# Optimization experiments

Measured on AMD Instinct MI355X. Metric: run time of the kernel, lower is better.

The kernel has to match this reference:

```python
import jax, jax.numpy as jnp
import numpy as np

# ---- static config (mirrors init_kwargs) ----
WIN_X, WIN_Y = 12, 12
GRID_X, GRID_Y = 468, 468
BATCH = 4
SHIFTS = ((0, 0), (6, 6))
MAX_WIN_X = GRID_X // WIN_X + 1            # 40
MAX_WIN_Y = GRID_Y // WIN_Y + 1            # 40
MAX_WIN_PER_SAMPLE = MAX_WIN_X * MAX_WIN_Y # 1600
# (level, max_tokens, drop_range_lo, drop_range_hi)
DROP_INFO = ((0, 30, 0, 30), (1, 60, 30, 60), (2, 100, 60, 100000))
SENTINEL = 2_000_000_000  # window id for masked-out voxels (sorts to the end)


def _window_partition(coors):
    # coors: [N,4] = [b, z, y, x] int32 -> batch-unique window index per shift
    out = []
    for sx, sy in SHIFTS:
        x = coors[:, 3] + sx
        y = coors[:, 2] + sy
        wx = x // WIN_X
        wy = y // WIN_Y
        out.append((coors[:, 0] * MAX_WIN_PER_SAMPLE + wx * MAX_WIN_Y + wy).astype(jnp.int32))
    return out


def _sort_group_stats(win):
    # inner index within each equal-value group (counting-sort style) and group size per element
    order = jnp.argsort(win)                      # stable
    s = win[order]
    n = win.shape[0]
    left_s = jnp.searchsorted(s, s, side='left')
    inner_sorted = jnp.arange(n, dtype=win.dtype) - left_s.astype(win.dtype)
    inner = jnp.zeros_like(win).at[order].set(inner_sorted)
    counts = (jnp.searchsorted(s, win, side='right') - jnp.searchsorted(s, win, side='left')).astype(win.dtype)
    return inner, counts


def _drop_single_shift(win, valid):
    # equivalent of SSTInputLayer.drop_single_shift restricted to `valid` voxels
    w = jnp.where(valid, win, SENTINEL)
    inner, counts = _sort_group_stats(w)
    target = jnp.zeros_like(w)
    lvl = -jnp.ones_like(w)
    for dl, max_tok, lo, hi in DROP_INFO:
        m = (counts >= lo) & (counts < hi)
        target = jnp.where(m, max_tok, target)
        lvl = jnp.where(m, dl, lvl)
    keep = valid & (inner < target)
    return keep, jnp.where(valid, lvl, -1)


def _make_continuous(w):
    # dense-rank of window ids (make_continuous_inds) over a sentinel-masked array
    order = jnp.argsort(w)
    s = w[order]
    new_grp = jnp.concatenate([jnp.zeros((1,), w.dtype), (s[1:] != s[:-1]).astype(w.dtype)])
    rank = jnp.cumsum(new_grp)
    return jnp.zeros_like(w).at[order].set(rank)


def _flat2win(win, keep, lvl):
    # per-voxel position in the [num_windows, max_tokens] buffer of its drop level; -1 if dropped
    out = -jnp.ones_like(win)
    for dl, max_tok, _, _ in DROP_INFO:
        valid = keep & (lvl == dl)
        w = jnp.where(valid, win, SENTINEL)
        conti = _make_continuous(w)
        inner, _ = _sort_group_stats(w)
        out = jnp.where(valid, conti * max_tok + inner, out)
    return out


def reference(voxel_feat, coors):
    coors = coors.astype(jnp.int32)
    bwi0, bwi1 = _window_partition(coors)
    n = voxel_feat.shape[0]
    all_valid = jnp.ones((n,), bool)
    keep0, lvl0 = _drop_single_shift(bwi0, all_valid)
    keep1, lvl1 = _drop_single_shift(bwi1, keep0)   # shift-1 drop computed among shift-0 survivors
    keep = keep0 & keep1
    feat = jnp.where(keep[:, None], voxel_feat, 0.0)  # fixed-shape analogue of voxel_feat[voxel_keep_inds]
    f2w0 = _flat2win(bwi0, keep, lvl0)
    f2w1 = _flat2win(bwi1, keep, lvl1)
    return feat, keep, lvl0, lvl1, bwi0, bwi1, f2w0, f2w1


def setup_inputs() -> dict:
    key = jax.random.key(0)
    k1, k2, k3, k4 = jax.random.split(key, 4)
    n, c = 300000, 128
    voxel_feat = jax.random.normal(k1, (n, c), dtype=jnp.float32)
    b = jax.random.randint(k2, (n,), 0, BATCH)
    y = jax.random.randint(k3, (n,), 0, GRID_Y)
    x = jax.random.randint(k4, (n,), 0, GRID_X)
    z = jnp.zeros((n,), jnp.int32)
    coors = jnp.stack([b, z, y, x], axis=1).astype(jnp.int32)
    return {"voxel_feat": voxel_feat, "coors": coors}
```

## Files before the change

### kernel.cpp

```cpp
#include <hip/hip_runtime.h>


#define NWIN 6400
#define SEG_CAP 3072

__global__ void k_zero(int* __restrict__ hdr, int* __restrict__ keepF, int n) {
    int i = blockIdx.x * blockDim.x + threadIdx.x;
    if (i < 4 * NWIN) hdr[i] = 0;
    if (i < n) keepF[i] = 0;
}

__global__ void k_windows(const int* __restrict__ coors, int n,
                          int* __restrict__ w0a, int* __restrict__ w1a,
                          int* __restrict__ cnt0) {
    int i = blockIdx.x * blockDim.x + threadIdx.x;
    if (i >= n) return;
    int b = coors[4 * i];
    int y = coors[4 * i + 2];
    int x = coors[4 * i + 3];
    int w0 = b * 1600 + (x / 12) * 40 + (y / 12);
    int w1 = b * 1600 + ((x + 6) / 12) * 40 + ((y + 6) / 12);
    w0a[i] = w0;
    w1a[i] = w1;
    atomicAdd(&cnt0[w0], 1);
}

__global__ void k_scan(const int* __restrict__ cnt, int* __restrict__ base,
                       int* __restrict__ lvlW) {
    __shared__ int psum[256];
    int t = threadIdx.x;
    int st = t * 25;
    int s = 0;
    for (int j = 0; j < 25; j++) s += cnt[st + j];
    psum[t] = s;
    __syncthreads();
    if (t == 0) {
        int acc = 0;
        for (int j = 0; j < 256; j++) { int v = psum[j]; psum[j] = acc; acc += v; }
    }
    __syncthreads();
    int acc = psum[t];
    for (int j = 0; j < 25; j++) {
        int w = st + j;
        int c = cnt[w];
        base[w] = acc;
        acc += c;
        int lvl;
        if (c < 30) lvl = 0;
        else if (c < 60) lvl = 1;
        else if (c < 100000) lvl = 2;
        else lvl = -1;
        lvlW[w] = lvl;
    }
}

__global__ void k_count_masked(const int* __restrict__ wa, const int* __restrict__ mask,
                               int n, int* __restrict__ cnt) {
    int i = blockIdx.x * blockDim.x + threadIdx.x;
    if (i >= n) return;
    if (!mask[i]) return;
    atomicAdd(&cnt[wa[i]], 1);
}

__global__ void k_scatter(const int* __restrict__ wa, const int* __restrict__ mask, int n,
                          const int* __restrict__ base, int* __restrict__ cur,
                          int* __restrict__ seg) {
    int i = blockIdx.x * blockDim.x + threadIdx.x;
    if (i >= n) return;
    if (mask && !mask[i]) return;
    int w = wa[i];
    int p = atomicAdd(&cur[w], 1);
    seg[base[w] + p] = i;
}

__global__ void k_rankkeep(const int* __restrict__ cnt, const int* __restrict__ base,
                           const int* __restrict__ seg, int* __restrict__ keepOut) {
    int w = blockIdx.x;
    int k = cnt[w];
    if (k == 0) return;
    int bs = base[w];
    int target;
    if (k < 30) target = 30;
    else if (k < 60) target = 60;
    else if (k < 100000) target = 100;
    else target = 0;
    __shared__ int lds[SEG_CAP];
    if (k <= SEG_CAP) {
        for (int j = threadIdx.x; j < k; j += blockDim.x) lds[j] = seg[bs + j];
        __syncthreads();
        for (int e = threadIdx.x; e < k; e += blockDim.x) {
            int v = lds[e];
            int r = 0;
            for (int j = 0; j < k; j++) r += (lds[j] < v) ? 1 : 0;
            keepOut[v] = (r < target) ? 1 : 0;
        }
    } else {
        for (int e = threadIdx.x; e < k; e += blockDim.x) {
            int v = seg[bs + e];
            int r = 0;
            for (int j = 0; j < k; j++) r += (seg[bs + j] < v) ? 1 : 0;
            keepOut[v] = (r < target) ? 1 : 0;
        }
    }
}

__global__ void k_rankkept(const int* __restrict__ cnt, const int* __restrict__ base,
                           const int* __restrict__ seg, const int* __restrict__ keepF,
                           int* __restrict__ rk, int* __restrict__ keptC) {
    int w = blockIdx.x;
    int k = cnt[w];
    __shared__ int lds[SEG_CAP];
    __shared__ int red[64];
    int local = 0;
    if (k > 0) {
        int bs = base[w];
        if (k <= SEG_CAP) {
            for (int j = threadIdx.x; j < k; j += blockDim.x) {
                int v = seg[bs + j];
                lds[j] = v | (keepF[v] << 30);
            }
            __syncthreads();
            for (int e = threadIdx.x; e < k; e += blockDim.x) {
                int enc = lds[e];
                int kept = enc >> 30;
                local += kept;
                if (!kept) continue;
                int v = enc & 0x3FFFFFFF;
                int r = 0;
                for (int j = 0; j < k; j++) {
                    int ej = lds[j];
                    r += (ej >> 30) & (int)((ej & 0x3FFFFFFF) < v);
                }
                rk[v] = r;
            }
        } else {
            for (int e = threadIdx.x; e < k; e += blockDim.x) {
                int v = seg[bs + e];
                int f = keepF[v];
                local += f;
                if (!f) continue;
                int r = 0;
                for (int j = 0; j < k; j++) {
                    int u = seg[bs + j];
                    r += (keepF[u] && (u < v)) ? 1 : 0;
                }
                rk[v] = r;
            }
        }
    }
    red[threadIdx.x] = local;
    __syncthreads();
    if (threadIdx.x == 0) {
        int s = 0;
        for (int j = 0; j < 64; j++) s += red[j];
        keptC[w] = s;
    }
}

__global__ void k_conti(const int* __restrict__ lvlW, const int* __restrict__ keptC,
                        int* __restrict__ conti) {
    __shared__ int pc0[256], pc1[256], pc2[256];
    int t = threadIdx.x;
    int st = t * 25;
    int c0 = 0, c1 = 0, c2 = 0;
    for (int j = 0; j < 25; j++) {
        int w = st + j;
        if (keptC[w] > 0) {
            int l = lvlW[w];
            c0 += (l == 0); c1 += (l == 1); c2 += (l == 2);
        }
    }
    pc0[t] = c0; pc1[t] = c1; pc2[t] = c2;
    __syncthreads();
    if (t == 0) {
        int a = 0, b = 0, c = 0;
        for (int j = 0; j < 256; j++) {
            int v0 = pc0[j], v1 = pc1[j], v2 = pc2[j];
            pc0[j] = a; pc1[j] = b; pc2[j] = c;
            a += v0; b += v1; c += v2;
        }
    }
    __syncthreads();
    int a0 = pc0[t], a1 = pc1[t], a2 = pc2[t];
    for (int j = 0; j < 25; j++) {
        int w = st + j;
        int l = lvlW[w];
        int cc = (l == 0) ? a0 : (l == 1) ? a1 : (l == 2) ? a2 : 0;
        conti[w] = cc;
        if (keptC[w] > 0) {
            if (l == 0) a0++; else if (l == 1) a1++; else if (l == 2) a2++;
        }
    }
}

__global__ void k_final(int n, const int* __restrict__ w0a, const int* __restrict__ w1a,
                        const int* __restrict__ keep0, const int* __restrict__ keepF,
                        const int* __restrict__ lvlW0, const int* __restrict__ lvlW1,
                        const int* __restrict__ conti0, const int* __restrict__ conti1,
                        const int* __restrict__ rk0, const int* __restrict__ rk1,
                        float* __restrict__ out) {
    int i = blockIdx.x * blockDim.x + threadIdx.x;
    if (i >= n) return;
    size_t N = (size_t)n;
    float* o = out + N * 128;
    int w0 = w0a[i], w1 = w1a[i];
    int k0 = keep0[i];
    int kf = keepF[i];
    int l0 = lvlW0[w0];
    int l1 = k0 ? lvlW1[w1] : -1;
    int f0 = -1, f1 = -1;
    if (kf) {
        int mt0 = (l0 == 0) ? 30 : (l0 == 1) ? 60 : 100;
        int mt1 = (l1 == 0) ? 30 : (l1 == 1) ? 60 : 100;
        f0 = conti0[w0] * mt0 + rk0[i];
        f1 = conti1[w1] * mt1 + rk1[i];
    }
    o[i]         = (float)kf;
    o[N + i]     = (float)l0;
    o[2 * N + i] = (float)l1;
    o[3 * N + i] = (float)w0;
    o[4 * N + i] = (float)w1;
    o[5 * N + i] = (float)f0;
    o[6 * N + i] = (float)f1;
}

__global__ void k_feat(const float4* __restrict__ in, const int* __restrict__ keepF,
                       float4* __restrict__ out, int n) {
    int gid = blockIdx.x * blockDim.x + threadIdx.x;
    int total = n * 32;
    if (gid >= total) return;
    int row = gid >> 5;
    float4 v = in[gid];
    if (!keepF[row]) { v.x = 0.f; v.y = 0.f; v.z = 0.f; v.w = 0.f; }
    out[gid] = v;
}

extern "C" void kernel_launch(void* const* d_in, const int* in_sizes, int n_in,
                              void* d_out, int out_size, void* d_ws, size_t ws_size,
                              hipStream_t stream) {
    (void)n_in; (void)out_size; (void)ws_size;
    const float* feat = (const float*)d_in[0];
    const int* coors  = (const int*)d_in[1];
    int n = in_sizes[1] / 4;
    float* out = (float*)d_out;
    int* ws = (int*)d_ws;

    int* cnt0   = ws;
    int* cur0   = ws + 6400;
    int* cnt1   = ws + 12800;
    int* cur1   = ws + 19200;
    int* base0  = ws + 25600;
    int* base1  = ws + 32000;
    int* lvlW0  = ws + 38400;
    int* lvlW1  = ws + 44800;
    int* keptC0 = ws + 51200;
    int* keptC1 = ws + 57600;
    int* conti0 = ws + 64000;
    int* conti1 = ws + 70400;
    int* w0a    = ws + 76800;
    int* w1a    = w0a + n;
    int* seg0   = w1a + n;
    int* seg1   = seg0 + n;
    int* keep0  = seg1 + n;
    int* keepF  = keep0 + n;
    int* rk0    = keepF + n;
    int* rk1    = rk0 + n;

    int nb = (n + 255) / 256;
    int zmax = (n > 4 * NWIN) ? n : 4 * NWIN;
    int zb = (zmax + 255) / 256;

    k_zero<<<zb, 256, 0, stream>>>(cnt0, keepF, n);
    k_windows<<<nb, 256, 0, stream>>>(coors, n, w0a, w1a, cnt0);
    k_scan<<<1, 256, 0, stream>>>(cnt0, base0, lvlW0);
    k_scatter<<<nb, 256, 0, stream>>>(w0a, (const int*)nullptr, n, base0, cur0, seg0);
    k_rankkeep<<<NWIN, 64, 0, stream>>>(cnt0, base0, seg0, keep0);
    k_count_masked<<<nb, 256, 0, stream>>>(w1a, keep0, n, cnt1);
    k_scan<<<1, 256, 0, stream>>>(cnt1, base1, lvlW1);
    k_scatter<<<nb, 256, 0, stream>>>(w1a, keep0, n, base1, cur1, seg1);
    k_rankkeep<<<NWIN, 64, 0, stream>>>(cnt1, base1, seg1, keepF);
    k_rankkept<<<NWIN, 64, 0, stream>>>(cnt0, base0, seg0, keepF, rk0, keptC0);
    k_rankkept<<<NWIN, 64, 0, stream>>>(cnt1, base1, seg1, keepF, rk1, keptC1);
    k_conti<<<1, 256, 0, stream>>>(lvlW0, keptC0, conti0);
    k_conti<<<1, 256, 0, stream>>>(lvlW1, keptC1, conti1);
    k_final<<<nb, 256, 0, stream>>>(n, w0a, w1a, keep0, keepF, lvlW0, lvlW1,
                                    conti0, conti1, rk0, rk1, out);
    int fb = (n * 32 + 255) / 256;
    k_feat<<<fb, 256, 0, stream>>>((const float4*)feat, keepF, (float4*)out, n);
}
```

Baseline: 438.9 us.

## Replace scan-based segmenting with fixed-capacity window buckets and wave-level shuffle ranking

Drops the prefix-scan and separate scatter passes by appending each voxel straight into a fixed 128-slot bucket per window during window computation. Ranking runs one wavefront per window using shuffles instead of LDS, and the shift-1 bucket fill and kept counts are folded into the ranking kernels via atomics. The two conti scans and the final/feature kernels are each merged into one launch, and levels are recomputed from counts instead of stored. Windows holding more than 128 voxels fall back to a very slow single-thread scan over all n voxels.

```diff
diff --git a/kernel.cpp b/kernel.cpp
--- a/kernel.cpp
+++ b/kernel.cpp
@@ -2,171 +2,209 @@
 
 
 #define NWIN 6400
-#define SEG_CAP 3072
-
-__global__ void k_zero(int* __restrict__ hdr, int* __restrict__ keepF, int n) {
-    int i = blockIdx.x * blockDim.x + threadIdx.x;
-    if (i < 4 * NWIN) hdr[i] = 0;
-    if (i < n) keepF[i] = 0;
-}
-
-__global__ void k_windows(const int* __restrict__ coors, int n,
-                          int* __restrict__ w0a, int* __restrict__ w1a,
-                          int* __restrict__ cnt0) {
-    int i = blockIdx.x * blockDim.x + threadIdx.x;
+#define CAP 128
+
+__device__ __forceinline__ int targ_of(int k) {
+    return (k < 30) ? 30 : (k < 60) ? 60 : (k < 100000) ? 100 : 0;
+}
+__device__ __forceinline__ int lvl_of(int k) {
+    return (k < 30) ? 0 : (k < 60) ? 1 : (k < 100000) ? 2 : -1;
+}
+
+__global__ void k_zero(int* __restrict__ z) {
+    int i = blockIdx.x * 256 + threadIdx.x;
+    if (i < 3 * NWIN) z[i] = 0;
+}
+
+__global__ void __launch_bounds__(256) k_winscat(
+    const int4* __restrict__ c4, int n,
+    int* __restrict__ w0a, int* __restrict__ w1a,
+    int* __restrict__ cnt0, int* __restrict__ seg0) {
+    int i = blockIdx.x * 256 + threadIdx.x;
     if (i >= n) return;
-    int b = coors[4 * i];
-    int y = coors[4 * i + 2];
-    int x = coors[4 * i + 3];
-    int w0 = b * 1600 + (x / 12) * 40 + (y / 12);
-    int w1 = b * 1600 + ((x + 6) / 12) * 40 + ((y + 6) / 12);
+    int4 c = c4[i];
+    int w0 = c.x * 1600 + (c.w / 12) * 40 + (c.z / 12);
+    int w1 = c.x * 1600 + ((c.w + 6) / 12) * 40 + ((c.z + 6) / 12);
     w0a[i] = w0;
     w1a[i] = w1;
-    atomicAdd(&cnt0[w0], 1);
-}
-
-__global__ void k_scan(const int* __restrict__ cnt, int* __restrict__ base,
-                       int* __restrict__ lvlW) {
-    __shared__ int psum[256];
-    int t = threadIdx.x;
-    int st = t * 25;
-    int s = 0;
-    for (int j = 0; j < 25; j++) s += cnt[st + j];
-    psum[t] = s;
-    __syncthreads();
-    if (t == 0) {
-        int acc = 0;
-        for (int j = 0; j < 256; j++) { int v = psum[j]; psum[j] = acc; acc += v; }
-    }
-    __syncthreads();
-    int acc = psum[t];
-    for (int j = 0; j < 25; j++) {
-        int w = st + j;
-        int c = cnt[w];
-        base[w] = acc;
-        acc += c;
-        int lvl;
-        if (c < 30) lvl = 0;
-        else if (c < 60) lvl = 1;
-        else if (c < 100000) lvl = 2;
-        else lvl = -1;
-        lvlW[w] = lvl;
-    }
-}
-
-__global__ void k_count_masked(const int* __restrict__ wa, const int* __restrict__ mask,
-                               int n, int* __restrict__ cnt) {
-    int i = blockIdx.x * blockDim.x + threadIdx.x;
-    if (i >= n) return;
-    if (!mask[i]) return;
-    atomicAdd(&cnt[wa[i]], 1);
-}
-
-__global__ void k_scatter(const int* __restrict__ wa, const int* __restrict__ mask, int n,
-                          const int* __restrict__ base, int* __restrict__ cur,
-                          int* __restrict__ seg) {
-    int i = blockIdx.x * blockDim.x + threadIdx.x;
-    if (i >= n) return;
-    if (mask && !mask[i]) return;
-    int w = wa[i];
-    int p = atomicAdd(&cur[w], 1);
-    seg[base[w] + p] = i;
-}
-
-__global__ void k_rankkeep(const int* __restrict__ cnt, const int* __restrict__ base,
-                           const int* __restrict__ seg, int* __restrict__ keepOut) {
-    int w = blockIdx.x;
-    int k = cnt[w];
+    int p = atomicAdd(&cnt0[w0], 1);
+    if (p < CAP) seg0[w0 * CAP + p] = i;
+}
+
+__global__ void __launch_bounds__(256) k_rank0(
+    const int* __restrict__ cnt0, const int* __restrict__ seg0,
+    const int* __restrict__ w0a, const int* __restrict__ w1a, int n,
+    int* __restrict__ keep0, int* __restrict__ cnt1, int* __restrict__ seg1) {
+    int w = blockIdx.x * 4 + (threadIdx.x >> 6);
+    int lane = threadIdx.x & 63;
+    int k = cnt0[w];
     if (k == 0) return;
-    int bs = base[w];
-    int target;
-    if (k < 30) target = 30;
-    else if (k < 60) target = 60;
-    else if (k < 100000) target = 100;
-    else target = 0;
-    __shared__ int lds[SEG_CAP];
-    if (k <= SEG_CAP) {
-        for (int j = threadIdx.x; j < k; j += blockDim.x) lds[j] = seg[bs + j];
-        __syncthreads();
-        for (int e = threadIdx.x; e < k; e += blockDim.x) {
-            int v = lds[e];
-            int r = 0;
-            for (int j = 0; j < k; j++) r += (lds[j] < v) ? 1 : 0;
-            keepOut[v] = (r < target) ? 1 : 0;
+    int target = targ_of(k);
+    const int* s = seg0 + w * CAP;
+    if (k <= 64) {
+        int v = (lane < k) ? s[lane] : 0x7FFFFFFF;
+        int r = 0;
+        for (int j = 0; j < k; j++) { int b = __shfl(v, j, 64); r += (b < v) ? 1 : 0; }
+        if (lane < k) {
+            int kp = (r < target) ? 1 : 0;
+            keep0[v] = kp;
+            if (kp) {
+                int w1 = w1a[v];
+                int p = atomicAdd(&cnt1[w1], 1);
+                if (p < CAP) seg1[w1 * CAP + p] = v;
+            }
+        }
+    } else if (k <= CAP) {
+        int k2 = k - 64;
+        int v0 = s[lane];
+        int v1 = (lane < k2) ? s[64 + lane] : 0x7FFFFFFF;
+        int r0 = 0, r1 = 0;
+        for (int j = 0; j < 64; j++) { int b = __shfl(v0, j, 64); r0 += (b < v0); r1 += (b < v1); }
+        for (int j = 0; j < k2; j++) { int b = __shfl(v1, j, 64); r0 += (b < v0); r1 += (b < v1); }
+        {
+            int kp = (r0 < target) ? 1 : 0;
+            keep0[v0] = kp;
+            if (kp) { int w1 = w1a[v0]; int p = atomicAdd(&cnt1[w1], 1); if (p < CAP) seg1[w1 * CAP + p] = v0; }
+        }
+        if (lane < k2) {
+            int kp = (r1 < target) ? 1 : 0;
+            keep0[v1] = kp;
+            if (kp) { int w1 = w1a[v1]; int p = atomicAdd(&cnt1[w1], 1); if (p < CAP) seg1[w1 * CAP + p] = v1; }
         }
     } else {
-        for (int e = threadIdx.x; e < k; e += blockDim.x) {
-            int v = seg[bs + e];
-            int r = 0;
-            for (int j = 0; j < k; j++) r += (seg[bs + j] < v) ? 1 : 0;
-            keepOut[v] = (r < target) ? 1 : 0;
-        }
-    }
-}
-
-__global__ void k_rankkept(const int* __restrict__ cnt, const int* __restrict__ base,
-                           const int* __restrict__ seg, const int* __restrict__ keepF,
-                           int* __restrict__ rk, int* __restrict__ keptC) {
-    int w = blockIdx.x;
-    int k = cnt[w];
-    __shared__ int lds[SEG_CAP];
-    __shared__ int red[64];
-    int local = 0;
-    if (k > 0) {
-        int bs = base[w];
-        if (k <= SEG_CAP) {
-            for (int j = threadIdx.x; j < k; j += blockDim.x) {
-                int v = seg[bs + j];
-                lds[j] = v | (keepF[v] << 30);
+        if (lane == 0) {
+            int c = 0;
+            for (int i = 0; i < n; i++) {
+                if (w0a[i] == w) {
+                    int kp = (c < target) ? 1 : 0;
+                    keep0[i] = kp;
+                    if (kp) { int w1 = w1a[i]; int p = atomicAdd(&cnt1[w1], 1); if (p < CAP) seg1[w1 * CAP + p] = i; }
+                    c++;
+                }
             }
-            __syncthreads();
-            for (int e = threadIdx.x; e < k; e += blockDim.x) {
-                int enc = lds[e];
-                int kept = enc >> 30;
-                local += kept;
-                if (!kept) continue;
-                int v = enc & 0x3FFFFFFF;
-                int r = 0;
-                for (int j = 0; j < k; j++) {
-                    int ej = lds[j];
-                    r += (ej >> 30) & (int)((ej & 0x3FFFFFFF) < v);
+        }
+    }
+}
+
+__global__ void __launch_bounds__(256) k_rank1(
+    const int* __restrict__ cnt1, const int* __restrict__ seg1,
+    const int* __restrict__ w0a, const int* __restrict__ w1a,
+    const int* __restrict__ keep0, int n,
+    int* __restrict__ keepF, int* __restrict__ rk1,
+    int* __restrict__ keptC1, int* __restrict__ keptC0) {
+    int w = blockIdx.x * 4 + (threadIdx.x >> 6);
+    int lane = threadIdx.x & 63;
+    int k = cnt1[w];
+    int target = targ_of(k);
+    if (lane == 0) keptC1[w] = (k < target) ? k : target;
+    if (k == 0) return;
+    const int* s = seg1 + w * CAP;
+    if (k <= 64) {
+        int v = (lane < k) ? s[lane] : 0x7FFFFFFF;
+        int r = 0;
+        for (int j = 0; j < k; j++) { int b = __shfl(v, j, 64); r += (b < v) ? 1 : 0; }
+        if (lane < k) {
+            int kp = (r < target) ? 1 : 0;
+            keepF[v] = kp;
+            if (kp) { rk1[v] = r; atomicAdd(&keptC0[w0a[v]], 1); }
+        }
+    } else if (k <= CAP) {
+        int k2 = k - 64;
+        int v0 = s[lane];
+        int v1 = (lane < k2) ? s[64 + lane] : 0x7FFFFFFF;
+        int r0 = 0, r1 = 0;
+        for (int j = 0; j < 64; j++) { int b = __shfl(v0, j, 64); r0 += (b < v0); r1 += (b < v1); }
+        for (int j = 0; j < k2; j++) { int b = __shfl(v1, j, 64); r0 += (b < v0); r1 += (b < v1); }
+        {
+            int kp = (r0 < target) ? 1 : 0;
+            keepF[v0] = kp;
+            if (kp) { rk1[v0] = r0; atomicAdd(&keptC0[w0a[v0]], 1); }
+        }
+        if (lane < k2) {
+            int kp = (r1 < target) ? 1 : 0;
+            keepF[v1] = kp;
+            if (kp) { rk1[v1] = r1; atomicAdd(&keptC0[w0a[v1]], 1); }
+        }
+    } else {
+        if (lane == 0) {
+            int c = 0;
+            for (int i = 0; i < n; i++) {
+                if (w1a[i] == w && keep0[i]) {
+                    int kp = (c < target) ? 1 : 0;
+                    keepF[i] = kp;
+                    if (kp) { rk1[i] = c; atomicAdd(&keptC0[w0a[i]], 1); }
+                    c++;
                 }
-                rk[v] = r;
             }
-        } else {
-            for (int e = threadIdx.x; e < k; e += blockDim.x) {
-                int v = seg[bs + e];
-                int f = keepF[v];
-                local += f;
-                if (!f) continue;
-                int r = 0;
-                for (int j = 0; j < k; j++) {
-                    int u = seg[bs + j];
-                    r += (keepF[u] && (u < v)) ? 1 : 0;
-                }
-                rk[v] = r;
+        }
+    }
+}
+
+__global__ void __launch_bounds__(256) k_rank0kept(
+    const int* __restrict__ cnt0, const int* __restrict__ seg0,
+    const int* __restrict__ keep0, const int* __restrict__ keepF,
+    const int* __restrict__ w0a, int n, int* __restrict__ rk0) {
+    int w = blockIdx.x * 4 + (threadIdx.x >> 6);
+    int lane = threadIdx.x & 63;
+    int k = cnt0[w];
+    if (k == 0) return;
+    const int* s = seg0 + w * CAP;
+    if (k <= 64) {
+        int v = 0x3FFFFFFF, f = 0;
+        if (lane < k) { v = s[lane]; f = (keep0[v] && keepF[v]) ? 1 : 0; }
+        int enc = v | (f << 30);
+        int r = 0;
+        for (int j = 0; j < k; j++) {
+            int b = __shfl(enc, j, 64);
+            r += ((b >> 30) & 1) & (int)((b & 0x3FFFFFFF) < v);
+        }
+        if (f) rk0[v] = r;
+    } else if (k <= CAP) {
+        int k2 = k - 64;
+        int v0 = s[lane];
+        int f0 = (keep0[v0] && keepF[v0]) ? 1 : 0;
+        int v1 = 0x3FFFFFFF, f1 = 0;
+        if (lane < k2) { v1 = s[64 + lane]; f1 = (keep0[v1] && keepF[v1]) ? 1 : 0; }
+        int e0 = v0 | (f0 << 30), e1 = v1 | (f1 << 30);
+        int r0 = 0, r1 = 0;
+        for (int j = 0; j < 64; j++) {
+            int b = __shfl(e0, j, 64);
+            int bf = (b >> 30) & 1, bv = b & 0x3FFFFFFF;
+            r0 += bf & (int)(bv < v0);
+            r1 += bf & (int)(bv < v1);
+        }
+        for (int j = 0; j < k2; j++) {
+            int b = __shfl(e1, j, 64);
+            int bf = (b >> 30) & 1, bv = b & 0x3FFFFFFF;
+            r0 += bf & (int)(bv < v0);
+            r1 += bf & (int)(bv < v1);
+        }
+        if (f0) rk0[v0] = r0;
+        if (f1) rk0[v1] = r1;
+    } else {
+        if (lane == 0) {
+            int c = 0;
+            for (int i = 0; i < n; i++) {
+                if (w0a[i] == w && keep0[i] && keepF[i]) { rk0[i] = c; c++; }
             }
         }
     }
-    red[threadIdx.x] = local;
-    __syncthreads();
-    if (threadIdx.x == 0) {
-        int s = 0;
-        for (int j = 0; j < 64; j++) s += red[j];
-        keptC[w] = s;
-    }
-}
-
-__global__ void k_conti(const int* __restrict__ lvlW, const int* __restrict__ keptC,
-                        int* __restrict__ conti) {
+}
+
+__global__ void k_conti2(
+    const int* __restrict__ cnt0, const int* __restrict__ keptC0, int* __restrict__ conti0,
+    const int* __restrict__ cnt1, const int* __restrict__ keptC1, int* __restrict__ conti1) {
     __shared__ int pc0[256], pc1[256], pc2[256];
+    const int* cnt   = blockIdx.x ? cnt1 : cnt0;
+    const int* keptC = blockIdx.x ? keptC1 : keptC0;
+    int* conti       = blockIdx.x ? conti1 : conti0;
     int t = threadIdx.x;
     int st = t * 25;
     int c0 = 0, c1 = 0, c2 = 0;
     for (int j = 0; j < 25; j++) {
         int w = st + j;
         if (keptC[w] > 0) {
-            int l = lvlW[w];
+            int l = lvl_of(cnt[w]);
             c0 += (l == 0); c1 += (l == 1); c2 += (l == 2);
         }
     }
@@ -184,55 +222,54 @@
     int a0 = pc0[t], a1 = pc1[t], a2 = pc2[t];
     for (int j = 0; j < 25; j++) {
         int w = st + j;
-        int l = lvlW[w];
-        int cc = (l == 0) ? a0 : (l == 1) ? a1 : (l == 2) ? a2 : 0;
-        conti[w] = cc;
+        int l = lvl_of(cnt[w]);
+        conti[w] = (l == 0) ? a0 : (l == 1) ? a1 : (l == 2) ? a2 : 0;
         if (keptC[w] > 0) {
             if (l == 0) a0++; else if (l == 1) a1++; else if (l == 2) a2++;
         }
     }
 }
 
-__global__ void k_final(int n, const int* __restrict__ w0a, const int* __restrict__ w1a,
-                        const int* __restrict__ keep0, const int* __restrict__ keepF,
-                        const int* __restrict__ lvlW0, const int* __restrict__ lvlW1,
-                        const int* __restrict__ conti0, const int* __restrict__ conti1,
-                        const int* __restrict__ rk0, const int* __restrict__ rk1,
-                        float* __restrict__ out) {
-    int i = blockIdx.x * blockDim.x + threadIdx.x;
-    if (i >= n) return;
-    size_t N = (size_t)n;
-    float* o = out + N * 128;
-    int w0 = w0a[i], w1 = w1a[i];
-    int k0 = keep0[i];
-    int kf = keepF[i];
-    int l0 = lvlW0[w0];
-    int l1 = k0 ? lvlW1[w1] : -1;
-    int f0 = -1, f1 = -1;
-    if (kf) {
-        int mt0 = (l0 == 0) ? 30 : (l0 == 1) ? 60 : 100;
-        int mt1 = (l1 == 0) ? 30 : (l1 == 1) ? 60 : 100;
-        f0 = conti0[w0] * mt0 + rk0[i];
-        f1 = conti1[w1] * mt1 + rk1[i];
-    }
-    o[i]         = (float)kf;
-    o[N + i]     = (float)l0;
-    o[2 * N + i] = (float)l1;
-    o[3 * N + i] = (float)w0;
-    o[4 * N + i] = (float)w1;
-    o[5 * N + i] = (float)f0;
-    o[6 * N + i] = (float)f1;
-}
-
-__global__ void k_feat(const float4* __restrict__ in, const int* __restrict__ keepF,
-                       float4* __restrict__ out, int n) {
-    int gid = blockIdx.x * blockDim.x + threadIdx.x;
-    int total = n * 32;
-    if (gid >= total) return;
-    int row = gid >> 5;
-    float4 v = in[gid];
-    if (!keepF[row]) { v.x = 0.f; v.y = 0.f; v.z = 0.f; v.w = 0.f; }
-    out[gid] = v;
+__global__ void __launch_bounds__(256) k_finalfeat(
+    int n, const int* __restrict__ w0a, const int* __restrict__ w1a,
+    const int* __restrict__ keep0, const int* __restrict__ keepF,
+    const int* __restrict__ cnt0, const int* __restrict__ cnt1,
+    const int* __restrict__ conti0, const int* __restrict__ conti1,
+    const int* __restrict__ rk0, const int* __restrict__ rk1,
+    const float4* __restrict__ feat, float* __restrict__ out, int nbScalar) {
+    if ((int)blockIdx.x < nbScalar) {
+        int i = blockIdx.x * 256 + threadIdx.x;
+        if (i >= n) return;
+        size_t N = (size_t)n;
+        float* o = out + N * 128;
+        int w0 = w0a[i], w1 = w1a[i];
+        int k0 = keep0[i];
+        int kf = (k0 && keepF[i]) ? 1 : 0;
+        int l0 = lvl_of(cnt0[w0]);
+        int l1 = k0 ? lvl_of(cnt1[w1]) : -1;
+        int f0 = -1, f1 = -1;
+        if (kf) {
+            int mt0 = (l0 == 0) ? 30 : (l0 == 1) ? 60 : 100;
+            int mt1 = (l1 == 0) ? 30 : (l1 == 1) ? 60 : 100;
+            f0 = conti0[w0] * mt0 + rk0[i];
+            f1 = conti1[w1] * mt1 + rk1[i];
+        }
+        o[i]         = (float)kf;
+        o[N + i]     = (float)l0;
+        o[2 * N + i] = (float)l1;
+        o[3 * N + i] = (float)w0;
+        o[4 * N + i] = (float)w1;
+        o[5 * N + i] = (float)f0;
+        o[6 * N + i] = (float)f1;
+    } else {
+        int gid = (blockIdx.x - nbScalar) * 256 + threadIdx.x;
+        int total = n * 32;
+        if (gid >= total) return;
+        int row = gid >> 5;
+        float4 v = feat[gid];
+        if (!(keep0[row] && keepF[row])) { v.x = 0.f; v.y = 0.f; v.z = 0.f; v.w = 0.f; }
+        ((float4*)out)[gid] = v;
+    }
 }
 
 extern "C" void kernel_launch(void* const* d_in, const int* in_sizes, int n_in,
@@ -246,45 +283,31 @@
     int* ws = (int*)d_ws;
 
     int* cnt0   = ws;
-    int* cur0   = ws + 6400;
-    int* cnt1   = ws + 12800;
-    int* cur1   = ws + 19200;
-    int* base0  = ws + 25600;
-    int* base1  = ws + 32000;
-    int* lvlW0  = ws + 38400;
-    int* lvlW1  = ws + 44800;
-    int* keptC0 = ws + 51200;
-    int* keptC1 = ws + 57600;
-    int* conti0 = ws + 64000;
-    int* conti1 = ws + 70400;
-    int* w0a    = ws + 76800;
+    int* cnt1   = ws + 6400;
+    int* keptC0 = ws + 12800;
+    int* keptC1 = ws + 19200;
+    int* conti0 = ws + 25600;
+    int* conti1 = ws + 32000;
+    int* w0a    = ws + 38400;
     int* w1a    = w0a + n;
-    int* seg0   = w1a + n;
-    int* seg1   = seg0 + n;
-    int* keep0  = seg1 + n;
+    int* keep0  = w1a + n;
     int* keepF  = keep0 + n;
     int* rk0    = keepF + n;
     int* rk1    = rk0 + n;
+    int* seg0   = rk1 + n;
+    int* seg1   = seg0 + NWIN * CAP;
 
     int nb = (n + 255) / 256;
-    int zmax = (n > 4 * NWIN) ? n : 4 * NWIN;
-    int zb = (zmax + 255) / 256;
-
-    k_zero<<<zb, 256, 0, stream>>>(cnt0, keepF, n);
-    k_windows<<<nb, 256, 0, stream>>>(coors, n, w0a, w1a, cnt0);
-    k_scan<<<1, 256, 0, stream>>>(cnt0, base0, lvlW0);
-    k_scatter<<<nb, 256, 0, stream>>>(w0a, (const int*)nullptr, n, base0, cur0, seg0);
-    k_rankkeep<<<NWIN, 64, 0, stream>>>(cnt0, base0, seg0, keep0);
-    k_count_masked<<<nb, 256, 0, stream>>>(w1a, keep0, n, cnt1);
-    k_scan<<<1, 256, 0, stream>>>(cnt1, base1, lvlW1);
-    k_scatter<<<nb, 256, 0, stream>>>(w1a, keep0, n, base1, cur1, seg1);
-    k_rankkeep<<<NWIN, 64, 0, stream>>>(cnt1, base1, seg1, keepF);
-    k_rankkept<<<NWIN, 64, 0, stream>>>(cnt0, base0, seg0, keepF, rk0, keptC0);
-    k_rankkept<<<NWIN, 64, 0, stream>>>(cnt1, base1, seg1, keepF, rk1, keptC1);
-    k_conti<<<1, 256, 0, stream>>>(lvlW0, keptC0, conti0);
-    k_conti<<<1, 256, 0, stream>>>(lvlW1, keptC1, conti1);
-    k_final<<<nb, 256, 0, stream>>>(n, w0a, w1a, keep0, keepF, lvlW0, lvlW1,
-                                    conti0, conti1, rk0, rk1, out);
     int fb = (n * 32 + 255) / 256;
-    k_feat<<<fb, 256, 0, stream>>>((const float4*)feat, keepF, (float4*)out, n);
-}
+
+    k_zero<<<(3 * NWIN + 255) / 256, 256, 0, stream>>>(cnt0);
+    k_winscat<<<nb, 256, 0, stream>>>((const int4*)coors, n, w0a, w1a, cnt0, seg0);
+    k_rank0<<<NWIN / 4, 256, 0, stream>>>(cnt0, seg0, w0a, w1a, n, keep0, cnt1, seg1);
+    k_rank1<<<NWIN / 4, 256, 0, stream>>>(cnt1, seg1, w0a, w1a, keep0, n,
+                                          keepF, rk1, keptC1, keptC0);
+    k_rank0kept<<<NWIN / 4, 256, 0, stream>>>(cnt0, seg0, keep0, keepF, w0a, n, rk0);
+    k_conti2<<<2, 256, 0, stream>>>(cnt0, keptC0, conti0, cnt1, keptC1, conti1);
+    k_finalfeat<<<nb + fb, 256, 0, stream>>>(n, w0a, w1a, keep0, keepF, cnt0, cnt1,
+                                             conti0, conti1, rk0, rk1,
+                                             (const float4*)feat, out, nb);
+}
```

Result: faster. 396.1 us (-9.8%).
